# Performance work log

Measured on AMD Instinct MI355X. Metric: run time of the kernel, lower is better.

## Reference

```python
import jax, jax.numpy as jnp
import numpy as np

REACH = 3
NEG_SLOPE = 0.01
NBINS = 256


def _conv(x, w, b=None):
    y = jax.lax.conv_general_dilated(x, w, (1, 1), 'VALID',
                                     dimension_numbers=('NCHW', 'OIHW', 'NCHW'))
    if b is not None:
        y = y + b[None, :, None, None]
    return y


def _causal_conv(x, wT, bT, wL, w1, b1, w2, b2, w3, b3):
    # top context: drop last row, pad (left=3,right=3,top=3), kernel (3,7) -> [N,32,H,W]
    xt = _conv(jnp.pad(x[:, :, :-1, :], ((0, 0), (0, 0), (REACH, 0), (REACH, REACH))), wT, bT)
    # left context: drop last col, pad left=3, kernel (1,3) -> [N,32,H,W]
    xl = _conv(jnp.pad(x[:, :, :, :-1], ((0, 0), (0, 0), (0, 0), (REACH, 0))), wL)
    h = jax.nn.leaky_relu(xt + xl, NEG_SLOPE)
    h = jax.nn.leaky_relu(_conv(h, w1, b1), NEG_SLOPE)
    h = jax.nn.leaky_relu(_conv(h, w2, b2), NEG_SLOPE)
    return jnp.clip(_conv(h, w3, b3), -1.0, 1.0)


def _pred_median3(x, a, b, c):
    med = jnp.maximum(jnp.minimum(a, jnp.maximum(b, c)), jnp.minimum(b, c))
    return jnp.fmod(x - med + 1.0, 2.0) - 1.0


def _calc_rmse(x):
    return 255.0 * jnp.sqrt(jnp.mean(jnp.square(x)))


def _calc_invCR(x):
    # x: [N,1,H,W]; per-channel 256-bin histogram over [-1,1], entropy in bits
    n = x.shape[0]
    res = x.shape[2] * x.shape[3]
    xf = x.reshape(n, res)
    idx = jnp.clip(jnp.floor((xf + 1.0) * (NBINS / 2.0)), 0, NBINS - 1).astype(jnp.int32)
    mask = ((xf >= -1.0) & (xf <= 1.0)).astype(xf.dtype)  # histc ignores out-of-range
    hist = jax.vmap(lambda i, m: jnp.zeros((NBINS,), xf.dtype).at[i].add(m))(idx, mask)
    p = hist / res
    ent = jnp.sum(jnp.where(p > 0, -p * jnp.log2(jnp.where(p > 0, p, 1.0)), 0.0))
    return ent / (8.0 * n)


def setup_inputs() -> dict:
    key = jax.random.key(0)
    ks = jax.random.split(key, 32)
    d = {}
    d['x'] = jax.random.uniform(ks[0], (4, 3, 512, 512), jnp.float32, -1.0, 1.0)
    i = 1
    for p in ['a', 'b', 'c']:
        d[p + '_wT'] = jax.random.normal(ks[i], (32, 1, 3, 7), jnp.float32) / np.float32(np.sqrt(21.0)); i += 1
        d[p + '_bT'] = jax.random.normal(ks[i], (32,), jnp.float32) * np.float32(0.01); i += 1
        d[p + '_wL'] = jax.random.normal(ks[i], (32, 1, 1, 3), jnp.float32) / np.float32(np.sqrt(3.0)); i += 1
        d[p + '_w1'] = jax.random.normal(ks[i], (32, 32, 1, 1), jnp.float32) / np.float32(np.sqrt(32.0)); i += 1
        d[p + '_b1'] = jax.random.normal(ks[i], (32,), jnp.float32) * np.float32(0.01); i += 1
        d[p + '_w2'] = jax.random.normal(ks[i], (32, 32, 1, 1), jnp.float32) / np.float32(np.sqrt(32.0)); i += 1
        d[p + '_b2'] = jax.random.normal(ks[i], (32,), jnp.float32) * np.float32(0.01); i += 1
        d[p + '_w3'] = jax.random.normal(ks[i], (1, 32, 1, 1), jnp.float32) / np.float32(np.sqrt(32.0)); i += 1
        d[p + '_b3'] = jax.random.normal(ks[i], (1,), jnp.float32) * np.float32(0.01); i += 1
    return d


def reference(x, a_wT, a_bT, a_wL, a_w1, a_b1, a_w2, a_b2, a_w3, a_b3,
              b_wT, b_bT, b_wL, b_w1, b_b1, b_w2, b_b2, b_w3, b_b3,
              c_wT, c_bT, c_wL, c_w1, c_b1, c_w2, c_b2, c_w3, c_b3):
    b, c, h, w = x.shape
    xr = x.reshape(b * c, 1, h, w)
    pa = _causal_conv(xr, a_wT, a_bT, a_wL, a_w1, a_b1, a_w2, a_b2, a_w3, a_b3)
    pb = _causal_conv(xr, b_wT, b_bT, b_wL, b_w1, b_b1, b_w2, b_b2, b_w3, b_b3)
    pc = _causal_conv(xr, c_wT, c_bT, c_wL, c_w1, c_b1, c_w2, c_b2, c_w3, c_b3)
    deltas = _pred_median3(xr, pa, pb, pc)
    loss1 = _calc_rmse(deltas)
    loss0 = _calc_rmse(xr)
    invCR0 = _calc_invCR(xr)
    invCR1 = _calc_invCR(deltas)
    return loss1, loss0, invCR0, invCR1
```

## Files before the change

kernel.cpp:

```cpp
#include <hip/hip_runtime.h>
#include <hip/hip_bf16.h>
#include <cmath>

#define HH 512
#define WW 512
#define NIMG 12
#define RES (HH*WW)
#define NBINS 256
#define PXB 512

typedef __attribute__((ext_vector_type(8))) short bf8;
typedef __attribute__((ext_vector_type(4))) float f32x4;
typedef __attribute__((ext_vector_type(2))) float f32x2;

__device__ __forceinline__ unsigned bf_rne(float x) {
    unsigned u = __float_as_uint(x);
    return (u + 0x7fffu + ((u >> 16) & 1u)) >> 16;
}

__device__ __forceinline__ unsigned cvtpk(float a, float b) {
    unsigned r;
    asm("v_cvt_pk_bf16_f32 %0, %1, %2" : "=v"(r) : "v"(a), "v"(b));
    return r;
}
__device__ __forceinline__ f32x2 pkmul(f32x2 a, f32x2 b) {
    f32x2 r;
    asm("v_pk_mul_f32 %0, %1, %2" : "=v"(r) : "v"(a), "v"(b));
    return r;
}

union bf8u { bf8 f; unsigned u[4]; };

__device__ __forceinline__ unsigned actpair(float x0, float x1, f32x2 k) {
    f32x2 a; a[0] = x0; a[1] = x1;
    const f32x2 p = pkmul(a, k);
    return cvtpk(fmaxf(x0, p[0]), fmaxf(x1, p[1]));
}

__device__ __forceinline__ bf8 actfrag(const f32x4 a0, const f32x4 a1, f32x2 k) {
    bf8u r;
    r.u[0] = actpair(a0[0], a0[1], k);
    r.u[1] = actpair(a0[2], a0[3], k);
    r.u[2] = actpair(a1[0], a1[1], k);
    r.u[3] = actpair(a1[2], a1[3], k);
    return r.f;
}

#define MFMA(A, B, C) __builtin_amdgcn_mfma_f32_16x16x32_bf16((A), (B), (C), 0, 0, 0)

__device__ __forceinline__ void run_pred_tile(
    const bf8 w0a, const bf8 w0b,
    const bf8 w1a, const bf8 w1b,
    const bf8 w2a, const bf8 w2b,
    const bf8 w3f,
    const f32x4 c10, const f32x4 c11, const f32x4 c20, const f32x4 c21,
    const bf8 pf, f32x4& acc3, const f32x2 k)
{
    const f32x4 z = {0.f, 0.f, 0.f, 0.f};
    f32x4 za = MFMA(w0a, pf, z);
    f32x4 zb = MFMA(w0b, pf, z);
    bf8 h = actfrag(za, zb, k);
    za = MFMA(w1a, h, c10);
    zb = MFMA(w1b, h, c11);
    h = actfrag(za, zb, k);
    za = MFMA(w2a, h, c20);
    zb = MFMA(w2b, h, c21);
    h = actfrag(za, zb, k);
    acc3 = MFMA(w3f, h, acc3);
}

__device__ __forceinline__ bf8 build_pf(const unsigned* __restrict__ rb, int tt, int q) {
    bf8u r;
    r.u[0] = rb[8*tt + 0];
    r.u[1] = rb[8*tt + 1];
    unsigned u2 = rb[8*tt + 2];
    unsigned u3 = rb[8*tt + 3];
    if (q == 3) { u2 = 0x00003f80u; u3 = 0u; }
    r.u[2] = u2; r.u[3] = u3;
    return r.f;
}

__global__ __launch_bounds__(192, 5) void codec_main(
    const float* __restrict__ x,
    const float* __restrict__ a_wT, const float* __restrict__ a_bT, const float* __restrict__ a_wL,
    const float* __restrict__ a_w1, const float* __restrict__ a_b1,
    const float* __restrict__ a_w2, const float* __restrict__ a_b2,
    const float* __restrict__ a_w3, const float* __restrict__ a_b3,
    const float* __restrict__ b_wT, const float* __restrict__ b_bT, const float* __restrict__ b_wL,
    const float* __restrict__ b_w1, const float* __restrict__ b_b1,
    const float* __restrict__ b_w2, const float* __restrict__ b_b2,
    const float* __restrict__ b_w3, const float* __restrict__ b_b3,
    const float* __restrict__ c_wT, const float* __restrict__ c_bT, const float* __restrict__ c_wL,
    const float* __restrict__ c_w1, const float* __restrict__ c_b1,
    const float* __restrict__ c_w2, const float* __restrict__ c_b2,
    const float* __restrict__ c_w3, const float* __restrict__ c_b3,
    float* __restrict__ sums,
    unsigned* __restrict__ hist_x,
    unsigned* __restrict__ hist_d)
{
    __shared__ unsigned rowbuf[4][2][260];
    __shared__ float predb[3][PXB];
    __shared__ unsigned shx[NBINS], shd[NBINS];
    __shared__ float red[8];

    const int tid  = threadIdx.x;
    const int lane = tid & 63;
    const int wv   = tid >> 6;
    const int q    = lane >> 4;
    const int m16  = lane & 15;

    for (int k = tid; k < NBINS; k += 192) { shx[k] = 0u; shd[k] = 0u; }

    const float* wT = (wv == 0) ? a_wT : ((wv == 1) ? b_wT : c_wT);
    const float* bT = (wv == 0) ? a_bT : ((wv == 1) ? b_bT : c_bT);
    const float* wL = (wv == 0) ? a_wL : ((wv == 1) ? b_wL : c_wL);
    const float* w1 = (wv == 0) ? a_w1 : ((wv == 1) ? b_w1 : c_w1);
    const float* b1 = (wv == 0) ? a_b1 : ((wv == 1) ? b_b1 : c_b1);
    const float* w2 = (wv == 0) ? a_w2 : ((wv == 1) ? b_w2 : c_w2);
    const float* b2 = (wv == 0) ? a_b2 : ((wv == 1) ? b_b2 : c_b2);
    const float* w3 = (wv == 0) ? a_w3 : ((wv == 1) ? b_w3 : c_w3);
    const float* b3 = (wv == 0) ? a_b3 : ((wv == 1) ? b_b3 : c_b3);

    bf8 wA0[2], wA1[2], wA2[2], aw3;
    f32x4 cb1[2], cb2[2];
    #pragma unroll
    for (int mt = 0; mt < 2; ++mt) {
        const int ch = ((m16 >> 2) << 3) + (mt << 2) + (m16 & 3);
        bf8 f0;
        #pragma unroll
        for (int j = 0; j < 8; ++j) {
            float v = 0.0f;
            if (q < 3) { if (j < 7) v = wT[ch*21 + q*7 + j]; }
            else       { if (j < 3) v = wL[ch*3 + j]; else if (j == 4) v = bT[ch]; }
            f0[j] = (short)bf_rne(v);
        }
        wA0[mt] = f0;
        {
            const f32x4 lo = *(const f32x4*)&w1[ch*32 + 8*q];
            const f32x4 hi = *(const f32x4*)&w1[ch*32 + 8*q + 4];
            bf8 g;
            #pragma unroll
            for (int j = 0; j < 4; ++j) { g[j] = (short)bf_rne(lo[j]); g[4+j] = (short)bf_rne(hi[j]); }
            wA1[mt] = g;
        }
        {
            const f32x4 lo = *(const f32x4*)&w2[ch*32 + 8*q];
            const f32x4 hi = *(const f32x4*)&w2[ch*32 + 8*q + 4];
            bf8 g;
            #pragma unroll
            for (int j = 0; j < 4; ++j) { g[j] = (short)bf_rne(lo[j]); g[4+j] = (short)bf_rne(hi[j]); }
            wA2[mt] = g;
        }
        if (mt == 0) { cb1[0] = *(const f32x4*)&b1[8*q];     cb2[0] = *(const f32x4*)&b2[8*q]; }
        else         { cb1[1] = *(const f32x4*)&b1[8*q + 4]; cb2[1] = *(const f32x4*)&b2[8*q + 4]; }
    }
    {
        bf8 g;
        #pragma unroll
        for (int j = 0; j < 8; ++j) {
            const float v = (m16 == 0) ? w3[8*q + j] : 0.0f;
            g[j] = (short)bf_rne(v);
        }
        aw3 = g;
    }
    f32x4 bias3v = {0.f, 0.f, 0.f, 0.f};
    if (q == 0) bias3v[0] = b3[0];

    f32x2 k001; k001[0] = 0.01f; k001[1] = 0.01f;

    const int img = blockIdx.y;
    const float* __restrict__ X = x + (size_t)img * RES;
    const int bx = blockIdx.x;
    const int i  = ((bx & 7) << 6) | (bx >> 3);

    for (int w = tid; w < 4*520; w += 192) {
        const int r   = w / 520;
        const int rem = w - r*520;
        const int cp  = rem / 260;
        const int wd  = rem - cp*260;
        const int srcrow = (r < 3) ? (i - 3 + r) : i;
        const int p0 = 2*wd - 4 + cp;
        float f0 = 0.0f, f1 = 0.0f;
        if (srcrow >= 0) {
            if ((unsigned)p0 < (unsigned)WW)       f0 = X[srcrow*WW + p0];
            if ((unsigned)(p0+1) < (unsigned)WW)   f1 = X[srcrow*WW + p0 + 1];
        }
        rowbuf[r][cp][wd] = cvtpk(f0, f1);
    }
    __syncthreads();

    const int cp = 1 - (m16 & 1);
    const int w0 = (m16 + 1) >> 1;
    const unsigned* __restrict__ rb = &rowbuf[q][cp][w0];

    #pragma unroll 1
    for (int u = 0; u < 8; ++u) {
        {
            const bf8 pfa = build_pf(rb, 4*u + 0, q);
            const bf8 pfb = build_pf(rb, 4*u + 1, q);
            f32x4 acc0 = bias3v, acc1 = bias3v;
            run_pred_tile(wA0[0], wA0[1], wA1[0], wA1[1], wA2[0], wA2[1], aw3,
                          cb1[0], cb1[1], cb2[0], cb2[1], pfa, acc0, k001);
            run_pred_tile(wA0[0], wA0[1], wA1[0], wA1[1], wA2[0], wA2[1], aw3,
                          cb1[0], cb1[1], cb2[0], cb2[1], pfb, acc1, k001);
            if (q == 0) {
                predb[wv][64*u      + m16] = fminf(fmaxf(acc0[0], -1.0f), 1.0f);
                predb[wv][64*u + 16 + m16] = fminf(fmaxf(acc1[0], -1.0f), 1.0f);
            }
        }
        {
            const bf8 pfa = build_pf(rb, 4*u + 2, q);
            const bf8 pfb = build_pf(rb, 4*u + 3, q);
            f32x4 acc0 = bias3v, acc1 = bias3v;
            run_pred_tile(wA0[0], wA0[1], wA1[0], wA1[1], wA2[0], wA2[1], aw3,
                          cb1[0], cb1[1], cb2[0], cb2[1], pfa, acc0, k001);
            run_pred_tile(wA0[0], wA0[1], wA1[0], wA1[1], wA2[0], wA2[1], aw3,
                          cb1[0], cb1[1], cb2[0], cb2[1], pfb, acc1, k001);
            if (q == 0) {
                predb[wv][64*u + 32 + m16] = fminf(fmaxf(acc0[0], -1.0f), 1.0f);
                predb[wv][64*u + 48 + m16] = fminf(fmaxf(acc1[0], -1.0f), 1.0f);
            }
        }
    }

    __syncthreads();

    float sx = 0.0f, sd = 0.0f;
    const float* __restrict__ Xrow = X + i*WW;
    for (int idx = tid; idx < PXB; idx += 192) {
        const float xv = Xrow[idx];
        const float pa = predb[0][idx];
        const float pb = predb[1][idx];
        const float pc = predb[2][idx];
        const float med = fmaxf(fminf(pa, fmaxf(pb, pc)), fminf(pb, pc));
        const float delta = fmodf(xv - med + 1.0f, 2.0f) - 1.0f;
        int bx2 = (int)floorf((xv + 1.0f) * 128.0f);
        bx2 = bx2 < 0 ? 0 : (bx2 > 255 ? 255 : bx2);
        if (xv >= -1.0f && xv <= 1.0f) atomicAdd(&shx[bx2], 1u);
        int bd = (int)floorf((delta + 1.0f) * 128.0f);
        bd = bd < 0 ? 0 : (bd > 255 ? 255 : bd);
        if (delta >= -1.0f && delta <= 1.0f) atomicAdd(&shd[bd], 1u);
        sx += xv*xv; sd += delta*delta;
    }

    #pragma unroll
    for (int off = 32; off > 0; off >>= 1) {
        sx += __shfl_down(sx, off);
        sd += __shfl_down(sd, off);
    }
    if (lane == 0) { red[wv] = sx; red[4 + wv] = sd; }
    __syncthreads();
    if (tid == 0) {
        atomicAdd(&sums[0], red[0] + red[1] + red[2]);
        atomicAdd(&sums[1], red[4] + red[5] + red[6]);
    }
    for (int k = tid; k < NBINS; k += 192) {
        if (shx[k]) atomicAdd(&hist_x[img*NBINS + k], shx[k]);
        if (shd[k]) atomicAdd(&hist_d[img*NBINS + k], shd[k]);
    }
}

__global__ __launch_bounds__(256) void codec_final(
    const float* __restrict__ sums,
    const unsigned* __restrict__ hist_x,
    const unsigned* __restrict__ hist_d,
    float* __restrict__ out)
{
    __shared__ float red[16];
    const int tid = threadIdx.x;
    float ex = 0.0f, ed = 0.0f;
    const float inv_res = 1.0f / (float)RES;
    for (int k = tid; k < NIMG*NBINS; k += 256) {
        const unsigned hx = hist_x[k];
        const unsigned hd = hist_d[k];
        if (hx) { const float p = (float)hx * inv_res; ex -= p * log2f(p); }
        if (hd) { const float p = (float)hd * inv_res; ed -= p * log2f(p); }
    }
    #pragma unroll
    for (int off = 32; off > 0; off >>= 1) {
        ex += __shfl_down(ex, off);
        ed += __shfl_down(ed, off);
    }
    const int lane = tid & 63, wv = tid >> 6;
    if (lane == 0) { red[wv] = ex; red[8 + wv] = ed; }
    __syncthreads();
    if (tid == 0) {
        const float Ex = red[0] + red[1] + red[2] + red[3];
        const float Ed = red[8] + red[9] + red[10] + red[11];
        const float inv_n = 1.0f / (float)(NIMG * RES);
        out[0] = 255.0f * sqrtf(sums[1] * inv_n);
        out[1] = 255.0f * sqrtf(sums[0] * inv_n);
        out[2] = Ex / (8.0f * (float)NIMG);
        out[3] = Ed / (8.0f * (float)NIMG);
    }
}

extern "C" void kernel_launch(void* const* d_in, const int* in_sizes, int n_in,
                              void* d_out, int out_size, void* d_ws, size_t ws_size,
                              hipStream_t stream)
{
    const float* x = (const float*)d_in[0];
    const float* w[27];
    for (int k = 0; k < 27; ++k) w[k] = (const float*)d_in[1 + k];

    float*    sums   = (float*)d_ws;
    unsigned* hist_x = (unsigned*)((char*)d_ws + 16);
    unsigned* hist_d = hist_x + NIMG*NBINS;
    const size_t zbytes = 16 + (size_t)2*NIMG*NBINS*sizeof(unsigned);
    hipMemsetAsync(d_ws, 0, zbytes, stream);

    dim3 grid(HH, NIMG);
    codec_main<<<grid, dim3(192), 0, stream>>>(
        x,
        w[0],  w[1],  w[2],  w[3],  w[4],  w[5],  w[6],  w[7],  w[8],
        w[9],  w[10], w[11], w[12], w[13], w[14], w[15], w[16], w[17],
        w[18], w[19], w[20], w[21], w[22], w[23], w[24], w[25], w[26],
        sums, hist_x, hist_d);
    codec_final<<<1, dim3(256), 0, stream>>>(sums, hist_x, hist_d, (float*)d_out);
}
```

Measured before the change: 320.5 us.

## Process two rows per block sharing a five-row staging buffer

Each block now predicts two consecutive image rows instead of one. It stages five source rows in LDS instead of four, so the overlapping context rows are loaded and converted once for both output rows, and the grid is halved. The fmodf in the residual wrap is replaced by a single conditional subtract. That is exact only while x - med + 1 stays in [-1, 3), which holds when x lies in [-1, 1]. The cost is more LDS per block (larger predb and rowbuf), which could limit how many blocks fit on a CU, and fewer, longer blocks.

```diff
diff --git a/kernel.cpp b/kernel.cpp
--- a/kernel.cpp
+++ b/kernel.cpp
@@ -7,7 +7,7 @@
 #define NIMG 12
 #define RES (HH*WW)
 #define NBINS 256
-#define PXB 512
+#define PXB 1024
 
 typedef __attribute__((ext_vector_type(8))) short bf8;
 typedef __attribute__((ext_vector_type(4))) float f32x4;
@@ -80,6 +80,8 @@
     return r.f;
 }
 
+#define RBW 260
+
 __global__ __launch_bounds__(192, 5) void codec_main(
     const float* __restrict__ x,
     const float* __restrict__ a_wT, const float* __restrict__ a_bT, const float* __restrict__ a_wL,
@@ -98,7 +100,7 @@
     unsigned* __restrict__ hist_x,
     unsigned* __restrict__ hist_d)
 {
-    __shared__ unsigned rowbuf[4][2][260];
+    __shared__ unsigned rowbuf[5][2][RBW];
     __shared__ float predb[3][PXB];
     __shared__ unsigned shx[NBINS], shd[NBINS];
     __shared__ float red[8];
@@ -171,14 +173,14 @@
     const int img = blockIdx.y;
     const float* __restrict__ X = x + (size_t)img * RES;
     const int bx = blockIdx.x;
-    const int i  = ((bx & 7) << 6) | (bx >> 3);
-
-    for (int w = tid; w < 4*520; w += 192) {
-        const int r   = w / 520;
-        const int rem = w - r*520;
-        const int cp  = rem / 260;
-        const int wd  = rem - cp*260;
-        const int srcrow = (r < 3) ? (i - 3 + r) : i;
+    const int i0 = (((bx & 7) << 5) | (bx >> 3)) << 1;
+
+    for (int w = tid; w < 5*2*RBW; w += 192) {
+        const int r   = w / (2*RBW);
+        const int rem = w - r*(2*RBW);
+        const int cp  = rem / RBW;
+        const int wd  = rem - cp*RBW;
+        const int srcrow = i0 - 3 + r;
         const int p0 = 2*wd - 4 + cp;
         float f0 = 0.0f, f1 = 0.0f;
         if (srcrow >= 0) {
@@ -191,34 +193,39 @@
 
     const int cp = 1 - (m16 & 1);
     const int w0 = (m16 + 1) >> 1;
-    const unsigned* __restrict__ rb = &rowbuf[q][cp][w0];
 
     #pragma unroll 1
-    for (int u = 0; u < 8; ++u) {
-        {
-            const bf8 pfa = build_pf(rb, 4*u + 0, q);
-            const bf8 pfb = build_pf(rb, 4*u + 1, q);
-            f32x4 acc0 = bias3v, acc1 = bias3v;
-            run_pred_tile(wA0[0], wA0[1], wA1[0], wA1[1], wA2[0], wA2[1], aw3,
-                          cb1[0], cb1[1], cb2[0], cb2[1], pfa, acc0, k001);
-            run_pred_tile(wA0[0], wA0[1], wA1[0], wA1[1], wA2[0], wA2[1], aw3,
-                          cb1[0], cb1[1], cb2[0], cb2[1], pfb, acc1, k001);
-            if (q == 0) {
-                predb[wv][64*u      + m16] = fminf(fmaxf(acc0[0], -1.0f), 1.0f);
-                predb[wv][64*u + 16 + m16] = fminf(fmaxf(acc1[0], -1.0f), 1.0f);
+    for (int r2 = 0; r2 < 2; ++r2) {
+        const unsigned* __restrict__ rb = &rowbuf[q + r2][cp][w0];
+        const int pb0 = r2 << 9;
+
+        #pragma unroll 1
+        for (int u = 0; u < 8; ++u) {
+            {
+                const bf8 pfa = build_pf(rb, 4*u + 0, q);
+                const bf8 pfb = build_pf(rb, 4*u + 1, q);
+                f32x4 acc0 = bias3v, acc1 = bias3v;
+                run_pred_tile(wA0[0], wA0[1], wA1[0], wA1[1], wA2[0], wA2[1], aw3,
+                              cb1[0], cb1[1], cb2[0], cb2[1], pfa, acc0, k001);
+                run_pred_tile(wA0[0], wA0[1], wA1[0], wA1[1], wA2[0], wA2[1], aw3,
+                              cb1[0], cb1[1], cb2[0], cb2[1], pfb, acc1, k001);
+                if (q == 0) {
+                    predb[wv][pb0 + 64*u      + m16] = fminf(fmaxf(acc0[0], -1.0f), 1.0f);
+                    predb[wv][pb0 + 64*u + 16 + m16] = fminf(fmaxf(acc1[0], -1.0f), 1.0f);
+                }
             }
-        }
-        {
-            const bf8 pfa = build_pf(rb, 4*u + 2, q);
-            const bf8 pfb = build_pf(rb, 4*u + 3, q);
-            f32x4 acc0 = bias3v, acc1 = bias3v;
-            run_pred_tile(wA0[0], wA0[1], wA1[0], wA1[1], wA2[0], wA2[1], aw3,
-                          cb1[0], cb1[1], cb2[0], cb2[1], pfa, acc0, k001);
-            run_pred_tile(wA0[0], wA0[1], wA1[0], wA1[1], wA2[0], wA2[1], aw3,
-                          cb1[0], cb1[1], cb2[0], cb2[1], pfb, acc1, k001);
-            if (q == 0) {
-                predb[wv][64*u + 32 + m16] = fminf(fmaxf(acc0[0], -1.0f), 1.0f);
-                predb[wv][64*u + 48 + m16] = fminf(fmaxf(acc1[0], -1.0f), 1.0f);
+            {
+                const bf8 pfa = build_pf(rb, 4*u + 2, q);
+                const bf8 pfb = build_pf(rb, 4*u + 3, q);
+                f32x4 acc0 = bias3v, acc1 = bias3v;
+                run_pred_tile(wA0[0], wA0[1], wA1[0], wA1[1], wA2[0], wA2[1], aw3,
+                              cb1[0], cb1[1], cb2[0], cb2[1], pfa, acc0, k001);
+                run_pred_tile(wA0[0], wA0[1], wA1[0], wA1[1], wA2[0], wA2[1], aw3,
+                              cb1[0], cb1[1], cb2[0], cb2[1], pfb, acc1, k001);
+                if (q == 0) {
+                    predb[wv][pb0 + 64*u + 32 + m16] = fminf(fmaxf(acc0[0], -1.0f), 1.0f);
+                    predb[wv][pb0 + 64*u + 48 + m16] = fminf(fmaxf(acc1[0], -1.0f), 1.0f);
+                }
             }
         }
     }
@@ -226,14 +233,15 @@
     __syncthreads();
 
     float sx = 0.0f, sd = 0.0f;
-    const float* __restrict__ Xrow = X + i*WW;
+    const float* __restrict__ Xrow = X + i0*WW;
     for (int idx = tid; idx < PXB; idx += 192) {
         const float xv = Xrow[idx];
         const float pa = predb[0][idx];
         const float pb = predb[1][idx];
         const float pc = predb[2][idx];
         const float med = fmaxf(fminf(pa, fmaxf(pb, pc)), fminf(pb, pc));
-        const float delta = fmodf(xv - med + 1.0f, 2.0f) - 1.0f;
+        const float v = xv - med + 1.0f;
+        const float delta = ((v >= 2.0f) ? v - 2.0f : v) - 1.0f;
         int bx2 = (int)floorf((xv + 1.0f) * 128.0f);
         bx2 = bx2 < 0 ? 0 : (bx2 > 255 ? 255 : bx2);
         if (xv >= -1.0f && xv <= 1.0f) atomicAdd(&shx[bx2], 1u);
@@ -309,7 +317,7 @@
     const size_t zbytes = 16 + (size_t)2*NIMG*NBINS*sizeof(unsigned);
     hipMemsetAsync(d_ws, 0, zbytes, stream);
 
-    dim3 grid(HH, NIMG);
+    dim3 grid(HH/2, NIMG);
     codec_main<<<grid, dim3(192), 0, stream>>>(
         x,
         w[0],  w[1],  w[2],  w[3],  w[4],  w[5],  w[6],  w[7],  w[8],
```

Measured after the change: 279.7 us. 12.7% less time.
